# Kernel optimization log

Measured on AMD Instinct MI355X. Metric: run time of the kernel, lower is better.

## Reference

```python
import jax, jax.numpy as jnp
import numpy as np

N, E, H, L, G = 50000, 500000, 128, 4, 1000
EPS = 1e-7      # GENConv message eps
LN_EPS = 1e-5   # torch LayerNorm default


def setup_inputs() -> dict:
    key = jax.random.key(0)
    ks = jax.random.split(key, 24)
    d = {}
    d["x"] = jax.random.normal(ks[0], (N, 9), jnp.float32)
    d["edge_index"] = jax.random.randint(ks[1], (2, E), 0, N, jnp.int32)
    d["edge_attr"] = jax.random.normal(ks[2], (E, 3), jnp.float32)
    d["batch"] = jnp.sort(jax.random.randint(ks[3], (N,), 0, G, jnp.int32))
    s9, s3, sh, s2h = 1/np.sqrt(9), 1/np.sqrt(3), 1/np.sqrt(H), 1/np.sqrt(2*H)
    u = lambda k, shp, s: jax.random.uniform(k, shp, jnp.float32, -s, s)
    d["enc_node_W"] = u(ks[4], (9, H), s9)
    d["enc_node_b"] = u(ks[5], (H,), s9)
    d["enc_edge_W"] = u(ks[6], (3, H), s3)
    d["enc_edge_b"] = u(ks[7], (H,), s3)
    d["ln_g"] = jnp.ones((L, H), jnp.float32)   # DeepGCNLayer pre-norm affine
    d["ln_b"] = jnp.zeros((L, H), jnp.float32)
    d["W1"] = u(ks[8], (L, H, 2*H), sh)          # GENConv MLP layer 1
    d["b1"] = u(ks[9], (L, 2*H), sh)
    d["mlp_ln_g"] = jnp.ones((L, 2*H), jnp.float32)
    d["mlp_ln_b"] = jnp.zeros((L, 2*H), jnp.float32)
    d["W2"] = u(ks[10], (L, 2*H, H), s2h)        # GENConv MLP layer 2
    d["b2"] = u(ks[11], (L, H), s2h)
    d["t"] = jnp.ones((L,), jnp.float32)         # learnable softmax temperature, init 1.0
    return d


def layernorm(x, g, b):
    mu = x.mean(-1, keepdims=True)
    var = ((x - mu) ** 2).mean(-1, keepdims=True)
    return (x - mu) / jnp.sqrt(var + LN_EPS) * g + b


def genconv(h, src, dst, ea, t, W1, b1, lg, lb, W2, b2):
    # message: relu(x_j + edge_attr) + eps   -> [E, H]
    msg = jax.nn.relu(h[src] + ea) + EPS
    # softmax aggregation over incoming edges, per channel
    logits = t * msg
    m = jax.ops.segment_max(logits, dst, num_segments=N)
    num = jnp.exp(logits - m[dst])
    den = jax.ops.segment_sum(num, dst, num_segments=N)
    alpha = num / den[dst]
    agg = jax.ops.segment_sum(msg * alpha, dst, num_segments=N)
    out = agg + h  # root residual inside GENConv
    z = jax.nn.relu(layernorm(out @ W1 + b1, lg, lb))
    return z @ W2 + b2


def reference(x, edge_index, edge_attr, batch, enc_node_W, enc_node_b,
              enc_edge_W, enc_edge_b, ln_g, ln_b, W1, b1, mlp_ln_g, mlp_ln_b,
              W2, b2, t):
    src, dst = edge_index[0], edge_index[1]
    h = x @ enc_node_W + enc_node_b            # node encoder  [N, H]
    ea = edge_attr @ enc_edge_W + enc_edge_b   # edge encoder  [E, H]
    # layer 0: conv only (DeeperGCN forward uses layers[0].conv directly)
    h = genconv(h, src, dst, ea, t[0], W1[0], b1[0], mlp_ln_g[0], mlp_ln_b[0], W2[0], b2[0])
    # layers 1..L-1: res+ block: x + conv(relu(LN(x))); dropout is identity (eval)
    for i in range(1, L):
        z = jax.nn.relu(layernorm(h, ln_g[i], ln_b[i]))
        h = h + genconv(z, src, dst, ea, t[i], W1[i], b1[i], mlp_ln_g[i], mlp_ln_b[i], W2[i], b2[i])
    h = jax.nn.relu(layernorm(h, ln_g[0], ln_b[0]))  # reuses layer-0 norm
    # global mean pool over graphs
    counts = jax.ops.segment_sum(jnp.ones((N,), h.dtype), batch, num_segments=G)
    sums = jax.ops.segment_sum(h, batch, num_segments=G)
    return sums / jnp.maximum(counts, 1.0)[:, None]
```

## Files before the change

### kernel.cpp

```cpp
#include <hip/hip_runtime.h>

#define NN 50000
#define NE 500000
#define HD 128
#define HD2 256
#define NL 4
#define NG 1000

constexpr float MSG_EPS = 1e-7f;
constexpr float LNEPS   = 1e-5f;

typedef float  f32x4  __attribute__((ext_vector_type(4)));
typedef __bf16 bf16x8 __attribute__((ext_vector_type(8)));

__device__ __forceinline__ unsigned short f2b(float f) {
    unsigned int u = __float_as_uint(f);
    unsigned int r = u + 0x7FFFu + ((u >> 16) & 1u);
    return (unsigned short)(r >> 16);
}
__device__ __forceinline__ float b2f(unsigned short h) {
    return __uint_as_float(((unsigned int)h) << 16);
}
__device__ __forceinline__ unsigned int pack2(float a, float b) {
    return (unsigned int)f2b(a) | ((unsigned int)f2b(b) << 16);
}

__global__ void k_encode_nodes(const float* __restrict__ x, const float* __restrict__ W,
                               const float* __restrict__ b, unsigned short* __restrict__ zb) {
    int n = blockIdx.x;
    int c = threadIdx.x;
    float xr[9];
#pragma unroll
    for (int k = 0; k < 9; k++) xr[k] = x[n * 9 + k];
    float acc = b[c];
#pragma unroll
    for (int k = 0; k < 9; k++) acc = fmaf(xr[k], W[k * HD + c], acc);
    zb[n * HD + c] = f2b(acc);
}

__global__ void k_prep(const float* __restrict__ W1, const float* __restrict__ W2,
                       unsigned short* __restrict__ W1T, unsigned short* __restrict__ W2T) {
    int idx = blockIdx.x * 256 + threadIdx.x;
    {
        int k = idx & 127, n = (idx >> 7) & 255, l = idx >> 15;
        W1T[idx] = f2b(W1[(l * 128 + k) * 256 + n]);
    }
    {
        int k = idx & 255, n = (idx >> 8) & 127, l = idx >> 15;
        W2T[idx] = f2b(W2[(l * 256 + k) * 128 + n]);
    }
}

__global__ void k_hist(const int* __restrict__ dst, int* __restrict__ counts) {
    int e = blockIdx.x * blockDim.x + threadIdx.x;
    if (e < NE) atomicAdd(&counts[dst[e]], 1);
}

#define SCAN_B 512
__global__ void k_scan1(const int* __restrict__ counts, int* __restrict__ incl,
                        int* __restrict__ bsum) {
    __shared__ int s[SCAN_B];
    int i = blockIdx.x * SCAN_B + threadIdx.x;
    int v = (i < NN) ? counts[i] : 0;
    s[threadIdx.x] = v;
    __syncthreads();
    for (int off = 1; off < SCAN_B; off <<= 1) {
        int t = (threadIdx.x >= off) ? s[threadIdx.x - off] : 0;
        __syncthreads();
        s[threadIdx.x] += t;
        __syncthreads();
    }
    if (i < NN) incl[i] = s[threadIdx.x];
    if (threadIdx.x == SCAN_B - 1) bsum[blockIdx.x] = s[threadIdx.x];
}

__global__ void k_scan2(const int* __restrict__ bsum, int* __restrict__ boff, int nb) {
    __shared__ int s[128];
    int v = (threadIdx.x < nb) ? bsum[threadIdx.x] : 0;
    s[threadIdx.x] = v;
    __syncthreads();
    for (int off = 1; off < 128; off <<= 1) {
        int t = (threadIdx.x >= off) ? s[threadIdx.x - off] : 0;
        __syncthreads();
        s[threadIdx.x] += t;
        __syncthreads();
    }
    if (threadIdx.x < nb) boff[threadIdx.x] = s[threadIdx.x] - v;
}

__global__ void k_scan3(const int* __restrict__ incl, const int* __restrict__ boff,
                        int* __restrict__ row_start) {
    int i = blockIdx.x * SCAN_B + threadIdx.x;
    if (i < NN) row_start[i + 1] = incl[i] + boff[blockIdx.x];
    if (i == 0) row_start[0] = 0;
}

__global__ void k_scatter(const int* __restrict__ src, const int* __restrict__ dst,
                          const float* __restrict__ eattr, const int* __restrict__ row_start,
                          int* __restrict__ cursor, float4* __restrict__ aperm) {
    int e = blockIdx.x * blockDim.x + threadIdx.x;
    if (e >= NE) return;
    int d = dst[e];
    int p = row_start[d] + atomicAdd(&cursor[d], 1);
    float4 v;
    v.x = eattr[e * 3 + 0];
    v.y = eattr[e * 3 + 1];
    v.z = eattr[e * 3 + 2];
    v.w = __int_as_float(src[e] << 6);
    aperm[p] = v;
}

__device__ __forceinline__ void edge_acc2(float4 a, unsigned int zz, float2 w0, float2 w1,
                                          float2 w2, float2 bb, float tv, float& num0,
                                          float& num1, float& wm0, float& wm1) {
    float zx = b2f((unsigned short)zz), zy = b2f((unsigned short)(zz >> 16));
    float eax = fmaf(a.x, w0.x, fmaf(a.y, w1.x, fmaf(a.z, w2.x, bb.x)));
    float eay = fmaf(a.x, w0.y, fmaf(a.y, w1.y, fmaf(a.z, w2.y, bb.y)));
    float mx = fmaxf(zx + eax, 0.f) + MSG_EPS;
    float my = fmaxf(zy + eay, 0.f) + MSG_EPS;
    float ex = __expf(tv * mx), ey = __expf(tv * my);
    num0 += ex;
    num1 += ey;
    wm0 = fmaf(mx, ex, wm0);
    wm1 = fmaf(my, ey, wm1);
}

__global__ __launch_bounds__(256) void k_aggregate(const unsigned short* __restrict__ zbin,
                                                   const float4* __restrict__ aperm,
                                                   const int* __restrict__ row_start,
                                                   const float* __restrict__ We,
                                                   const float* __restrict__ be,
                                                   const float* __restrict__ t, int layer,
                                                   unsigned int* __restrict__ outb) {
    int w = threadIdx.x >> 6, lane = threadIdx.x & 63;
    int n = blockIdx.x * 4 + w;
    if (n >= NN) return;
    int c = lane * 2;
    float2 w0 = *(const float2*)&We[c];
    float2 w1 = *(const float2*)&We[HD + c];
    float2 w2 = *(const float2*)&We[2 * HD + c];
    float2 bb = *(const float2*)&be[c];
    float tv = t[layer];
    int s0 = row_start[n], s1 = row_start[n + 1];
    const unsigned int* z32 = (const unsigned int*)zbin;
    unsigned int zn = z32[(size_t)n * 64 + lane];
    float num0 = 0.f, num1 = 0.f, wm0 = 0.f, wm1 = 0.f;
    int p = s0;
    if (p + 4 <= s1) {
        float4 A0 = aperm[p], A1 = aperm[p + 1], A2 = aperm[p + 2], A3 = aperm[p + 3];
        for (; p + 8 <= s1; p += 4) {
            unsigned int g0 = z32[(unsigned int)__float_as_int(A0.w) + lane];
            unsigned int g1 = z32[(unsigned int)__float_as_int(A1.w) + lane];
            unsigned int g2 = z32[(unsigned int)__float_as_int(A2.w) + lane];
            unsigned int g3 = z32[(unsigned int)__float_as_int(A3.w) + lane];
            float4 B0 = aperm[p + 4], B1 = aperm[p + 5], B2 = aperm[p + 6],
                   B3 = aperm[p + 7];
            edge_acc2(A0, g0, w0, w1, w2, bb, tv, num0, num1, wm0, wm1);
            edge_acc2(A1, g1, w0, w1, w2, bb, tv, num0, num1, wm0, wm1);
            edge_acc2(A2, g2, w0, w1, w2, bb, tv, num0, num1, wm0, wm1);
            edge_acc2(A3, g3, w0, w1, w2, bb, tv, num0, num1, wm0, wm1);
            A0 = B0;
            A1 = B1;
            A2 = B2;
            A3 = B3;
        }
        {
            unsigned int g0 = z32[(unsigned int)__float_as_int(A0.w) + lane];
            unsigned int g1 = z32[(unsigned int)__float_as_int(A1.w) + lane];
            unsigned int g2 = z32[(unsigned int)__float_as_int(A2.w) + lane];
            unsigned int g3 = z32[(unsigned int)__float_as_int(A3.w) + lane];
            edge_acc2(A0, g0, w0, w1, w2, bb, tv, num0, num1, wm0, wm1);
            edge_acc2(A1, g1, w0, w1, w2, bb, tv, num0, num1, wm0, wm1);
            edge_acc2(A2, g2, w0, w1, w2, bb, tv, num0, num1, wm0, wm1);
            edge_acc2(A3, g3, w0, w1, w2, bb, tv, num0, num1, wm0, wm1);
            p += 4;
        }
    }
    for (; p < s1; p++) {
        float4 a = aperm[p];
        unsigned int zz = z32[(unsigned int)__float_as_int(a.w) + lane];
        edge_acc2(a, zz, w0, w1, w2, bb, tv, num0, num1, wm0, wm1);
    }
    float ox = ((s1 > s0) ? (wm0 / num0) : 0.f) + b2f((unsigned short)zn);
    float oy = ((s1 > s0) ? (wm1 / num1) : 0.f) + b2f((unsigned short)(zn >> 16));
    outb[(size_t)n * 64 + lane] = pack2(ox, oy);
}

#define BM 32
#define HS_LD 264
#define HT_LD 136

__global__ __launch_bounds__(256) void k_mlp(const unsigned short* __restrict__ outb,
                                             const unsigned short* __restrict__ W1T,
                                             const float* __restrict__ b1l,
                                             const float* __restrict__ lgl,
                                             const float* __restrict__ lbl,
                                             const unsigned short* __restrict__ W2T,
                                             const float* __restrict__ b2l,
                                             unsigned short* __restrict__ h,
                                             const float* __restrict__ gn,
                                             const float* __restrict__ bn,
                                             unsigned short* __restrict__ zb,
                                             int add_residual, int store_h) {
    __shared__ __align__(16) unsigned short Hs[BM * HS_LD];
    __shared__ __align__(16) unsigned short Ht[BM * HT_LD];
    __shared__ __align__(16) float2 st1[2][16][4];

    int nb = blockIdx.x * BM;
    int tid = threadIdx.x;
    int w = tid >> 6, lane = tid & 63, q = lane >> 4, i = lane & 15;

    bf16x8 areg[2][4];
#pragma unroll
    for (int rt = 0; rt < 2; rt++) {
        int row = nb + rt * 16 + i;
#pragma unroll
        for (int ks = 0; ks < 4; ks++)
            areg[rt][ks] = (row < NN)
                               ? *(const bf16x8*)&outb[(size_t)row * HD + ks * 32 + q * 8]
                               : (bf16x8)(__bf16)0.f;
    }

    unsigned int hv[8];
    const unsigned int* h32c = (const unsigned int*)h;
    if (add_residual) {
#pragma unroll
        for (int it = 0; it < 8; it++) {
            int row = nb + w + it * 4;
            hv[it] = (row < NN) ? h32c[(size_t)row * 64 + lane] : 0u;
        }
    } else {
#pragma unroll
        for (int it = 0; it < 8; it++) hv[it] = 0u;
    }
    float2 gg = *(const float2*)&gn[lane * 2];
    float2 cc = *(const float2*)&bn[lane * 2];

    f32x4 acc[2][4];
#pragma unroll
    for (int rt = 0; rt < 2; rt++)
#pragma unroll
        for (int ct = 0; ct < 4; ct++) acc[rt][ct] = (f32x4){0.f, 0.f, 0.f, 0.f};

    bf16x8 bcur[4];
#pragma unroll
    for (int ct = 0; ct < 4; ct++)
        bcur[ct] = *(const bf16x8*)&W1T[(w * 64 + ct * 16 + i) * HD + q * 8];

#pragma unroll
    for (int ks = 0; ks < 4; ks++) {
        bf16x8 bnxt[4];
        if (ks < 3) {
#pragma unroll
            for (int ct = 0; ct < 4; ct++)
                bnxt[ct] =
                    *(const bf16x8*)&W1T[(w * 64 + ct * 16 + i) * HD + (ks + 1) * 32 + q * 8];
        }
#pragma unroll
        for (int rt = 0; rt < 2; rt++)
#pragma unroll
            for (int ct = 0; ct < 4; ct++)
                acc[rt][ct] = __builtin_amdgcn_mfma_f32_16x16x32_bf16(areg[rt][ks], bcur[ct],
                                                                     acc[rt][ct], 0, 0, 0);
        if (ks < 3) {
#pragma unroll
            for (int ct = 0; ct < 4; ct++) bcur[ct] = bnxt[ct];
        }
    }

#pragma unroll
    for (int ct = 0; ct < 4; ct++) {
        float bb = b1l[w * 64 + ct * 16 + i];
#pragma unroll
        for (int rt = 0; rt < 2; rt++)
#pragma unroll
            for (int r = 0; r < 4; r++) acc[rt][ct][r] += bb;
    }

    {
        float sv[2][4], qv[2][4];
#pragma unroll
        for (int rt = 0; rt < 2; rt++)
#pragma unroll
            for (int r = 0; r < 4; r++) {
                float s = acc[rt][0][r] + acc[rt][1][r] + acc[rt][2][r] + acc[rt][3][r];
                float sq = 0.f;
#pragma unroll
                for (int ct = 0; ct < 4; ct++) sq = fmaf(acc[rt][ct][r], acc[rt][ct][r], sq);
                sv[rt][r] = s;
                qv[rt][r] = sq;
            }
#pragma unroll
        for (int m = 1; m <= 8; m <<= 1)
#pragma unroll
            for (int rt = 0; rt < 2; rt++)
#pragma unroll
                for (int r = 0; r < 4; r++) {
                    sv[rt][r] += __shfl_xor(sv[rt][r], m);
                    qv[rt][r] += __shfl_xor(qv[rt][r], m);
                }
        if (i == 0) {
#pragma unroll
            for (int rt = 0; rt < 2; rt++)
#pragma unroll
                for (int r = 0; r < 4; r++)
                    st1[rt][q * 4 + r][w] = make_float2(sv[rt][r], qv[rt][r]);
        }
    }
    __syncthreads();

    {
        float mu[2][4], inv[2][4];
#pragma unroll
        for (int rt = 0; rt < 2; rt++)
#pragma unroll
            for (int r = 0; r < 4; r++) {
                const float4* sp = (const float4*)&st1[rt][q * 4 + r][0];
                float4 a = sp[0], b = sp[1];
                float S = a.x + a.z + b.x + b.z;
                float Q = a.y + a.w + b.y + b.w;
                float m_ = S * (1.f / 256.f);
                float v_ = Q * (1.f / 256.f) - m_ * m_;
                mu[rt][r] = m_;
                inv[rt][r] = rsqrtf(v_ + LNEPS);
            }
#pragma unroll
        for (int ct = 0; ct < 4; ct++) {
            float g = lgl[w * 64 + ct * 16 + i];
            float c = lbl[w * 64 + ct * 16 + i];
#pragma unroll
            for (int rt = 0; rt < 2; rt++)
#pragma unroll
                for (int r = 0; r < 4; r++) {
                    float v =
                        fmaxf(fmaf((acc[rt][ct][r] - mu[rt][r]) * inv[rt][r], g, c), 0.f);
                    Hs[(rt * 16 + q * 4 + r) * HS_LD + w * 64 + ct * 16 + i] = f2b(v);
                }
        }
    }
    __syncthreads();

    f32x4 acc2[2][2];
#pragma unroll
    for (int rt = 0; rt < 2; rt++)
#pragma unroll
        for (int ct = 0; ct < 2; ct++) acc2[rt][ct] = (f32x4){0.f, 0.f, 0.f, 0.f};

    bf16x8 hc[2], bc[2];
#pragma unroll
    for (int rt = 0; rt < 2; rt++) hc[rt] = *(const bf16x8*)&Hs[(rt * 16 + i) * HS_LD + q * 8];
#pragma unroll
    for (int ct = 0; ct < 2; ct++)
        bc[ct] = *(const bf16x8*)&W2T[(w * 32 + ct * 16 + i) * HD2 + q * 8];

#pragma unroll
    for (int ks = 0; ks < 8; ks++) {
        bf16x8 hn[2], bn2[2];
        if (ks < 7) {
#pragma unroll
            for (int rt = 0; rt < 2; rt++)
                hn[rt] = *(const bf16x8*)&Hs[(rt * 16 + i) * HS_LD + (ks + 1) * 32 + q * 8];
#pragma unroll
            for (int ct = 0; ct < 2; ct++)
                bn2[ct] =
                    *(const bf16x8*)&W2T[(w * 32 + ct * 16 + i) * HD2 + (ks + 1) * 32 + q * 8];
        }
#pragma unroll
        for (int rt = 0; rt < 2; rt++)
#pragma unroll
            for (int ct = 0; ct < 2; ct++)
                acc2[rt][ct] = __builtin_amdgcn_mfma_f32_16x16x32_bf16(hc[rt], bc[ct],
                                                                      acc2[rt][ct], 0, 0, 0);
        if (ks < 7) {
#pragma unroll
            for (int rt = 0; rt < 2; rt++) hc[rt] = hn[rt];
#pragma unroll
            for (int ct = 0; ct < 2; ct++) bc[ct] = bn2[ct];
        }
    }

#pragma unroll
    for (int ct = 0; ct < 2; ct++) {
        float bb = b2l[w * 32 + ct * 16 + i];
#pragma unroll
        for (int rt = 0; rt < 2; rt++)
#pragma unroll
            for (int r = 0; r < 4; r++)
                Ht[(rt * 16 + q * 4 + r) * HT_LD + w * 32 + ct * 16 + i] =
                    f2b(acc2[rt][ct][r] + bb);
    }
    __syncthreads();

    {
        const unsigned int* Ht32 = (const unsigned int*)Ht;
        unsigned int* h32 = (unsigned int*)h;
        unsigned int* zb32 = (unsigned int*)zb;
#pragma unroll
        for (int it = 0; it < 8; it++) {
            int rr = w + it * 4;
            int row = nb + rr;
            unsigned int tv = Ht32[rr * (HT_LD / 2) + lane];
            float cx = b2f((unsigned short)tv) + b2f((unsigned short)hv[it]);
            float cy = b2f((unsigned short)(tv >> 16)) + b2f((unsigned short)(hv[it] >> 16));
            float s = cx + cy, sq = cx * cx + cy * cy;
#pragma unroll
            for (int m = 32; m >= 1; m >>= 1) {
                s += __shfl_xor(s, m);
                sq += __shfl_xor(sq, m);
            }
            float mu = s * (1.f / 128.f);
            float var = sq * (1.f / 128.f) - mu * mu;
            float inv = rsqrtf(var + LNEPS);
            float z0 = fmaxf(fmaf((cx - mu) * inv, gg.x, cc.x), 0.f);
            float z1 = fmaxf(fmaf((cy - mu) * inv, gg.y, cc.y), 0.f);
            if (row < NN) {
                if (store_h) h32[(size_t)row * 64 + lane] = pack2(cx, cy);
                zb32[(size_t)row * 64 + lane] = pack2(z0, z1);
            }
        }
    }
}

__global__ void k_gbounds(const int* __restrict__ batch, int* __restrict__ gstart) {
    int g = blockIdx.x * blockDim.x + threadIdx.x;
    if (g > NG) return;
    int lo = 0, hi = NN;
    while (lo < hi) {
        int mid = (lo + hi) >> 1;
        if (batch[mid] < g) lo = mid + 1;
        else hi = mid;
    }
    gstart[g] = lo;
}

__global__ void k_pool(const unsigned short* __restrict__ zb, const int* __restrict__ gstart,
                       float* __restrict__ out) {
    int g = blockIdx.x;
    int c = threadIdx.x;
    int a = gstart[g], b = gstart[g + 1];
    float s0 = 0.f, s1 = 0.f;
    int n = a;
    for (; n + 2 <= b; n += 2) {
        s0 += b2f(zb[(size_t)n * HD + c]);
        s1 += b2f(zb[(size_t)(n + 1) * HD + c]);
    }
    if (n < b) s0 += b2f(zb[(size_t)n * HD + c]);
    out[g * HD + c] = (s0 + s1) / fmaxf((float)(b - a), 1.f);
}

extern "C" void kernel_launch(void* const* d_in, const int* in_sizes, int n_in, void* d_out,
                              int out_size, void* d_ws, size_t ws_size, hipStream_t stream) {
    const float* x     = (const float*)d_in[0];
    const int* ei      = (const int*)d_in[1];
    const float* eattr = (const float*)d_in[2];
    const int* batch   = (const int*)d_in[3];
    const float* encW  = (const float*)d_in[4];
    const float* encB  = (const float*)d_in[5];
    const float* eW    = (const float*)d_in[6];
    const float* eB    = (const float*)d_in[7];
    const float* ln_g  = (const float*)d_in[8];
    const float* ln_b  = (const float*)d_in[9];
    const float* W1    = (const float*)d_in[10];
    const float* b1    = (const float*)d_in[11];
    const float* mlg   = (const float*)d_in[12];
    const float* mlb   = (const float*)d_in[13];
    const float* W2    = (const float*)d_in[14];
    const float* b2    = (const float*)d_in[15];
    const float* t     = (const float*)d_in[16];
    const int* src = ei;
    const int* dst = ei + NE;

    char* w = (char*)d_ws;
    auto alloc = [&](size_t bytes) {
        char* p = w;
        w += (bytes + 255) & ~size_t(255);
        return p;
    };
    unsigned short* h    = (unsigned short*)alloc(sizeof(unsigned short) * NN * HD);
    unsigned short* zb   = (unsigned short*)alloc(sizeof(unsigned short) * NN * HD);
    unsigned int* outb   = (unsigned int*)alloc(sizeof(unsigned int) * NN * HD / 2);
    float4* aperm        = (float4*)alloc(sizeof(float4) * NE);
    int* row_start       = (int*)alloc(sizeof(int) * (NN + 1));
    int* counts          = (int*)alloc(sizeof(int) * NN);
    int* cursor          = (int*)alloc(sizeof(int) * NN);
    int* incl            = (int*)alloc(sizeof(int) * NN);
    int* bsum            = (int*)alloc(sizeof(int) * 128);
    int* boff            = (int*)alloc(sizeof(int) * 128);
    int* gstart          = (int*)alloc(sizeof(int) * (NG + 1));
    unsigned short* W1T  = (unsigned short*)alloc(sizeof(unsigned short) * NL * HD * HD2);
    unsigned short* W2T  = (unsigned short*)alloc(sizeof(unsigned short) * NL * HD2 * HD);

    hipMemsetAsync(counts, 0, sizeof(int) * NN, stream);
    hipMemsetAsync(cursor, 0, sizeof(int) * NN, stream);

    k_prep<<<512, 256, 0, stream>>>(W1, W2, W1T, W2T);
    k_encode_nodes<<<NN, HD, 0, stream>>>(x, encW, encB, zb);
    k_hist<<<(NE + 255) / 256, 256, 0, stream>>>(dst, counts);
    int nsb = (NN + SCAN_B - 1) / SCAN_B;
    k_scan1<<<nsb, SCAN_B, 0, stream>>>(counts, incl, bsum);
    k_scan2<<<1, 128, 0, stream>>>(bsum, boff, nsb);
    k_scan3<<<nsb, SCAN_B, 0, stream>>>(incl, boff, row_start);
    k_scatter<<<(NE + 255) / 256, 256, 0, stream>>>(src, dst, eattr, row_start, cursor, aperm);
    k_gbounds<<<(NG + 256) / 256, 256, 0, stream>>>(batch, gstart);

    for (int l = 0; l < NL; l++) {
        k_aggregate<<<(NN + 3) / 4, 256, 0, stream>>>(zb, aperm, row_start, eW, eB, t, l, outb);
        int ln_next = (l + 1) % NL;
        k_mlp<<<(NN + BM - 1) / BM, 256, 0, stream>>>(
            (const unsigned short*)outb, W1T + (size_t)l * HD * HD2, b1 + l * HD2,
            mlg + l * HD2, mlb + l * HD2, W2T + (size_t)l * HD2 * HD, b2 + l * HD, h,
            ln_g + ln_next * HD, ln_b + ln_next * HD, zb, l > 0, l < NL - 1);
    }
    k_pool<<<NG, HD, 0, stream>>>(zb, gstart, (float*)d_out);
}
```

Baseline: 490.3 us.

## Enlarge MLP tile to 64 rows with 8 waves and LDS-staged A operand

Doubles the k_mlp row tile to 64 nodes and the block to 512 threads (8 waves). Each wave now covers a narrower column slice of W1/W2, so weight fragments are reused across four row tiles instead of two. The input activations are staged through shared memory instead of per-wave register loads, and that buffer is reused for the output tile. The explicit register double-buffering of B fragments is dropped, and a larger LDS footprint may lower occupancy.

After: 502.9 us. 2.6% more time.

```diff
diff --git a/kernel.cpp b/kernel.cpp
--- a/kernel.cpp
+++ b/kernel.cpp
@@ -186,47 +186,36 @@
     outb[(size_t)n * 64 + lane] = pack2(ox, oy);
 }
 
-#define BM 32
+#define BM 64
 #define HS_LD 264
-#define HT_LD 136
-
-__global__ __launch_bounds__(256) void k_mlp(const unsigned short* __restrict__ outb,
-                                             const unsigned short* __restrict__ W1T,
-                                             const float* __restrict__ b1l,
-                                             const float* __restrict__ lgl,
-                                             const float* __restrict__ lbl,
-                                             const unsigned short* __restrict__ W2T,
-                                             const float* __restrict__ b2l,
-                                             unsigned short* __restrict__ h,
-                                             const float* __restrict__ gn,
-                                             const float* __restrict__ bn,
-                                             unsigned short* __restrict__ zb,
-                                             int add_residual, int store_h) {
+#define AS_W 68
+
+__global__ __launch_bounds__(512, 4) void k_mlp(const unsigned short* __restrict__ outb,
+                                                const unsigned short* __restrict__ W1T,
+                                                const float* __restrict__ b1l,
+                                                const float* __restrict__ lgl,
+                                                const float* __restrict__ lbl,
+                                                const unsigned short* __restrict__ W2T,
+                                                const float* __restrict__ b2l,
+                                                unsigned short* __restrict__ h,
+                                                const float* __restrict__ gn,
+                                                const float* __restrict__ bn,
+                                                unsigned short* __restrict__ zb,
+                                                int add_residual, int store_h) {
     __shared__ __align__(16) unsigned short Hs[BM * HS_LD];
-    __shared__ __align__(16) unsigned short Ht[BM * HT_LD];
-    __shared__ __align__(16) float2 st1[2][16][4];
+    __shared__ __align__(16) unsigned int AsHt[BM * AS_W];
+    __shared__ __align__(16) float2 st1[4][16][8];
 
     int nb = blockIdx.x * BM;
     int tid = threadIdx.x;
     int w = tid >> 6, lane = tid & 63, q = lane >> 4, i = lane & 15;
 
-    bf16x8 areg[2][4];
-#pragma unroll
-    for (int rt = 0; rt < 2; rt++) {
-        int row = nb + rt * 16 + i;
-#pragma unroll
-        for (int ks = 0; ks < 4; ks++)
-            areg[rt][ks] = (row < NN)
-                               ? *(const bf16x8*)&outb[(size_t)row * HD + ks * 32 + q * 8]
-                               : (bf16x8)(__bf16)0.f;
-    }
-
     unsigned int hv[8];
     const unsigned int* h32c = (const unsigned int*)h;
     if (add_residual) {
 #pragma unroll
         for (int it = 0; it < 8; it++) {
-            int row = nb + w + it * 4;
+            int row = nb + w + it * 8;
             hv[it] = (row < NN) ? h32c[(size_t)row * 64 + lane] : 0u;
         }
     } else {
@@ -236,64 +225,68 @@
     float2 gg = *(const float2*)&gn[lane * 2];
     float2 cc = *(const float2*)&bn[lane * 2];
 
-    f32x4 acc[2][4];
-#pragma unroll
-    for (int rt = 0; rt < 2; rt++)
-#pragma unroll
-        for (int ct = 0; ct < 4; ct++) acc[rt][ct] = (f32x4){0.f, 0.f, 0.f, 0.f};
-
-    bf16x8 bcur[4];
-#pragma unroll
-    for (int ct = 0; ct < 4; ct++)
-        bcur[ct] = *(const bf16x8*)&W1T[(w * 64 + ct * 16 + i) * HD + q * 8];
+    {
+        const float4* src = (const float4*)outb;
+        int r0 = tid >> 4, slot = tid & 15;
+#pragma unroll
+        for (int it = 0; it < 2; it++) {
+            int r = r0 + it * 32;
+            int row = nb + r;
+            float4 v = (row < NN) ? src[(size_t)row * 16 + slot]
+                                  : make_float4(0.f, 0.f, 0.f, 0.f);
+            *(float4*)&AsHt[r * AS_W + slot * 4] = v;
+        }
+    }
+    __syncthreads();
+
+    f32x4 acc[4][2];
+#pragma unroll
+    for (int rt = 0; rt < 4; rt++)
+#pragma unroll
+        for (int ct = 0; ct < 2; ct++) acc[rt][ct] = (f32x4){0.f, 0.f, 0.f, 0.f};
 
 #pragma unroll
     for (int ks = 0; ks < 4; ks++) {
-        bf16x8 bnxt[4];
-        if (ks < 3) {
-#pragma unroll
-            for (int ct = 0; ct < 4; ct++)
-                bnxt[ct] =
-                    *(const bf16x8*)&W1T[(w * 64 + ct * 16 + i) * HD + (ks + 1) * 32 + q * 8];
-        }
-#pragma unroll
-        for (int rt = 0; rt < 2; rt++)
-#pragma unroll
-            for (int ct = 0; ct < 4; ct++)
-                acc[rt][ct] = __builtin_amdgcn_mfma_f32_16x16x32_bf16(areg[rt][ks], bcur[ct],
+        bf16x8 av[4], bv[2];
+#pragma unroll
+        for (int rt = 0; rt < 4; rt++)
+            av[rt] = *(const bf16x8*)&AsHt[(rt * 16 + i) * AS_W + ks * 16 + q * 4];
+#pragma unroll
+        for (int ct = 0; ct < 2; ct++)
+            bv[ct] = *(const bf16x8*)&W1T[(w * 32 + ct * 16 + i) * HD + ks * 32 + q * 8];
+#pragma unroll
+        for (int rt = 0; rt < 4; rt++)
+#pragma unroll
+            for (int ct = 0; ct < 2; ct++)
+                acc[rt][ct] = __builtin_amdgcn_mfma_f32_16x16x32_bf16(av[rt], bv[ct],
                                                                      acc[rt][ct], 0, 0, 0);
-        if (ks < 3) {
-#pragma unroll
-            for (int ct = 0; ct < 4; ct++) bcur[ct] = bnxt[ct];
-        }
-    }
-
-#pragma unroll
-    for (int ct = 0; ct < 4; ct++) {
-        float bb = b1l[w * 64 + ct * 16 + i];
-#pragma unroll
-        for (int rt = 0; rt < 2; rt++)
+    }
+
+#pragma unroll
+    for (int ct = 0; ct < 2; ct++) {
+        float bb = b1l[w * 32 + ct * 16 + i];
+#pragma unroll
+        for (int rt = 0; rt < 4; rt++)
 #pragma unroll
             for (int r = 0; r < 4; r++) acc[rt][ct][r] += bb;
     }
 
     {
-        float sv[2][4], qv[2][4];
-#pragma unroll
-        for (int rt = 0; rt < 2; rt++)
+        float sv[4][4], qv[4][4];
+#pragma unroll
+        for (int rt = 0; rt < 4; rt++)
 #pragma unroll
             for (int r = 0; r < 4; r++) {
-                float s = acc[rt][0][r] + acc[rt][1][r] + acc[rt][2][r] + acc[rt][3][r];
-                float sq = 0.f;
-#pragma unroll
-                for (int ct = 0; ct < 4; ct++) sq = fmaf(acc[rt][ct][r], acc[rt][ct][r], sq);
+                float s = acc[rt][0][r] + acc[rt][1][r];
+                float sq = fmaf(acc[rt][0][r], acc[rt][0][r],
+                                acc[rt][1][r] * acc[rt][1][r]);
                 sv[rt][r] = s;
                 qv[rt][r] = sq;
             }
 #pragma unroll
         for (int m = 1; m <= 8; m <<= 1)
 #pragma unroll
-            for (int rt = 0; rt < 2; rt++)
+            for (int rt = 0; rt < 4; rt++)
 #pragma unroll
                 for (int r = 0; r < 4; r++) {
                     sv[rt][r] += __shfl_xor(sv[rt][r], m);
@@ -301,7 +294,7 @@
                 }
         if (i == 0) {
 #pragma unroll
-            for (int rt = 0; rt < 2; rt++)
+            for (int rt = 0; rt < 4; rt++)
 #pragma unroll
                 for (int r = 0; r < 4; r++)
                     st1[rt][q * 4 + r][w] = make_float2(sv[rt][r], qv[rt][r]);
@@ -310,96 +303,72 @@
     __syncthreads();
 
     {
-        float mu[2][4], inv[2][4];
-#pragma unroll
-        for (int rt = 0; rt < 2; rt++)
+        float mu[4][4], inv[4][4];
+#pragma unroll
+        for (int rt = 0; rt < 4; rt++)
 #pragma unroll
             for (int r = 0; r < 4; r++) {
                 const float4* sp = (const float4*)&st1[rt][q * 4 + r][0];
-                float4 a = sp[0], b = sp[1];
-                float S = a.x + a.z + b.x + b.z;
-                float Q = a.y + a.w + b.y + b.w;
+                float4 a = sp[0], b = sp[1], c4 = sp[2], d4 = sp[3];
+                float S = a.x + a.z + b.x + b.z + c4.x + c4.z + d4.x + d4.z;
+                float Q = a.y + a.w + b.y + b.w + c4.y + c4.w + d4.y + d4.w;
                 float m_ = S * (1.f / 256.f);
                 float v_ = Q * (1.f / 256.f) - m_ * m_;
                 mu[rt][r] = m_;
                 inv[rt][r] = rsqrtf(v_ + LNEPS);
             }
 #pragma unroll
-        for (int ct = 0; ct < 4; ct++) {
-            float g = lgl[w * 64 + ct * 16 + i];
-            float c = lbl[w * 64 + ct * 16 + i];
-#pragma unroll
-            for (int rt = 0; rt < 2; rt++)
+        for (int ct = 0; ct < 2; ct++) {
+            float g = lgl[w * 32 + ct * 16 + i];
+            float c = lbl[w * 32 + ct * 16 + i];
+#pragma unroll
+            for (int rt = 0; rt < 4; rt++)
 #pragma unroll
                 for (int r = 0; r < 4; r++) {
                     float v =
                         fmaxf(fmaf((acc[rt][ct][r] - mu[rt][r]) * inv[rt][r], g, c), 0.f);
-                    Hs[(rt * 16 + q * 4 + r) * HS_LD + w * 64 + ct * 16 + i] = f2b(v);
+                    Hs[(rt * 16 + q * 4 + r) * HS_LD + w * 32 + ct * 16 + i] = f2b(v);
                 }
         }
     }
     __syncthreads();
 
-    f32x4 acc2[2][2];
-#pragma unroll
-    for (int rt = 0; rt < 2; rt++)
-#pragma unroll
-        for (int ct = 0; ct < 2; ct++) acc2[rt][ct] = (f32x4){0.f, 0.f, 0.f, 0.f};
-
-    bf16x8 hc[2], bc[2];
-#pragma unroll
-    for (int rt = 0; rt < 2; rt++) hc[rt] = *(const bf16x8*)&Hs[(rt * 16 + i) * HS_LD + q * 8];
-#pragma unroll
-    for (int ct = 0; ct < 2; ct++)
-        bc[ct] = *(const bf16x8*)&W2T[(w * 32 + ct * 16 + i) * HD2 + q * 8];
+    f32x4 acc2[4];
+#pragma unroll
+    for (int rt = 0; rt < 4; rt++) acc2[rt] = (f32x4){0.f, 0.f, 0.f, 0.f};
 
 #pragma unroll
     for (int ks = 0; ks < 8; ks++) {
-        bf16x8 hn[2], bn2[2];
-        if (ks < 7) {
-#pragma unroll
-            for (int rt = 0; rt < 2; rt++)
-                hn[rt] = *(const bf16x8*)&Hs[(rt * 16 + i) * HS_LD + (ks + 1) * 32 + q * 8];
-#pragma unroll
-            for (int ct = 0; ct < 2; ct++)
-                bn2[ct] =
-                    *(const bf16x8*)&W2T[(w * 32 + ct * 16 + i) * HD2 + (ks + 1) * 32 + q * 8];
-        }
-#pragma unroll
-        for (int rt = 0; rt < 2; rt++)
-#pragma unroll
-            for (int ct = 0; ct < 2; ct++)
-                acc2[rt][ct] = __builtin_amdgcn_mfma_f32_16x16x32_bf16(hc[rt], bc[ct],
-                                                                      acc2[rt][ct], 0, 0, 0);
-        if (ks < 7) {
-#pragma unroll
-            for (int rt = 0; rt < 2; rt++) hc[rt] = hn[rt];
-#pragma unroll
-            for (int ct = 0; ct < 2; ct++) bc[ct] = bn2[ct];
-        }
-    }
-
-#pragma unroll
-    for (int ct = 0; ct < 2; ct++) {
-        float bb = b2l[w * 32 + ct * 16 + i];
-#pragma unroll
-        for (int rt = 0; rt < 2; rt++)
+        bf16x8 hc[4];
+#pragma unroll
+        for (int rt = 0; rt < 4; rt++)
+            hc[rt] = *(const bf16x8*)&Hs[(rt * 16 + i) * HS_LD + ks * 32 + q * 8];
+        bf16x8 bc = *(const bf16x8*)&W2T[(w * 16 + i) * HD2 + ks * 32 + q * 8];
+#pragma unroll
+        for (int rt = 0; rt < 4; rt++)
+            acc2[rt] = __builtin_amdgcn_mfma_f32_16x16x32_bf16(hc[rt], bc, acc2[rt], 0, 0, 0);
+    }
+
+    {
+        unsigned short* Ht = (unsigned short*)AsHt;
+        float bb = b2l[w * 16 + i];
+#pragma unroll
+        for (int rt = 0; rt < 4; rt++)
 #pragma unroll
             for (int r = 0; r < 4; r++)
-                Ht[(rt * 16 + q * 4 + r) * HT_LD + w * 32 + ct * 16 + i] =
-                    f2b(acc2[rt][ct][r] + bb);
-    }
-    __syncthreads();
-
-    {
-        const unsigned int* Ht32 = (const unsigned int*)Ht;
+                Ht[(rt * 16 + q * 4 + r) * (2 * AS_W) + w * 16 + i] = f2b(acc2[rt][r] + bb);
+    }
+    __syncthreads();
+
+    {
+        const unsigned int* Ht32 = AsHt;
         unsigned int* h32 = (unsigned int*)h;
         unsigned int* zb32 = (unsigned int*)zb;
 #pragma unroll
         for (int it = 0; it < 8; it++) {
-            int rr = w + it * 4;
+            int rr = w + it * 8;
             int row = nb + rr;
-            unsigned int tv = Ht32[rr * (HT_LD / 2) + lane];
+            unsigned int tv = Ht32[rr * AS_W + lane];
             float cx = b2f((unsigned short)tv) + b2f((unsigned short)hv[it]);
             float cy = b2f((unsigned short)(tv >> 16)) + b2f((unsigned short)(hv[it] >> 16));
             float s = cx + cy, sq = cx * cx + cy * cy;
@@ -506,7 +475,7 @@
     for (int l = 0; l < NL; l++) {
         k_aggregate<<<(NN + 3) / 4, 256, 0, stream>>>(zb, aperm, row_start, eW, eB, t, l, outb);
         int ln_next = (l + 1) % NL;
-        k_mlp<<<(NN + BM - 1) / BM, 256, 0, stream>>>(
+        k_mlp<<<(NN + BM - 1) / BM, 512, 0, stream>>>(
             (const unsigned short*)outb, W1T + (size_t)l * HD * HD2, b1 + l * HD2,
             mlg + l * HD2, mlb + l * HD2, W2T + (size_t)l * HD2 * HD, b2 + l * HD, h,
             ln_g + ln_next * HD, ln_b + ln_next * HD, zb, l > 0, l < NL - 1);
```
